# Kernel optimization log

Measured on AMD Instinct MI355X. Metric: run time of the kernel, lower is better.

The kernel has to match this reference:

```python
import jax, jax.numpy as jnp
import numpy as np

C = 256
NUM_HEADS = 4
GROUPS = 8
EPS = 1e-5


def setup_inputs() -> dict:
    key = jax.random.key(0)
    ks = jax.random.split(key, 7)
    B, H, W = 4, 64, 64
    x = jax.random.normal(ks[0], (B, C, H, W), dtype=jnp.float32)
    # GroupNorm affine params
    norm_w = jnp.ones((C,), dtype=jnp.float32)
    norm_b = jnp.zeros((C,), dtype=jnp.float32)
    # 1x1 convs == channel-mixing matrices
    qkv_w = jax.random.normal(ks[1], (3 * C, C), dtype=jnp.float32) * (C ** -0.5)
    qkv_b = jnp.zeros((3 * C,), dtype=jnp.float32)
    proj_w = jax.random.normal(ks[2], (C, C), dtype=jnp.float32) * (C ** -0.5)
    proj_b = jnp.zeros((C,), dtype=jnp.float32)
    return {"x": x, "norm_w": norm_w, "norm_b": norm_b,
            "qkv_w": qkv_w, "qkv_b": qkv_b,
            "proj_w": proj_w, "proj_b": proj_b}


def _group_norm(x, w, b):
    B, Cc, H, W = x.shape
    xr = x.reshape(B, GROUPS, Cc // GROUPS, H * W)
    mean = xr.mean(axis=(2, 3), keepdims=True)
    var = xr.var(axis=(2, 3), keepdims=True)
    xn = ((xr - mean) * jax.lax.rsqrt(var + EPS)).reshape(B, Cc, H, W)
    return xn * w[None, :, None, None] + b[None, :, None, None]


def reference(x, norm_w, norm_b, qkv_w, qkv_b, proj_w, proj_b):
    B, Cc, H, W = x.shape
    nh = NUM_HEADS
    d = Cc // nh
    h = _group_norm(x, norm_w, norm_b)
    # 1x1 conv: channel matmul
    qkv = jnp.einsum('oc,bchw->bohw', qkv_w, h) + qkv_b[None, :, None, None]
    q, k, v = jnp.split(qkv, 3, axis=1)
    q = q.reshape(B, nh, d, H * W)
    k = k.reshape(B, nh, d, H * W)
    v = v.reshape(B, nh, d, H * W)
    scale = d ** -0.5
    attn = jnp.einsum('bhci,bhcj->bhij', q, k) * scale  # [B, nh, HW, HW]
    attn = jax.nn.softmax(attn, axis=-1)
    o = jnp.einsum('bhij,bhcj->bhci', attn, v).reshape(B, Cc, H, W)
    out = jnp.einsum('oc,bchw->bohw', proj_w, o) + proj_b[None, :, None, None]
    return x + out
```

## Files before the change

### kernel.cpp

```cpp
#include <hip/hip_runtime.h>

typedef unsigned short u16;
typedef __attribute__((ext_vector_type(8))) short bf16x8;
typedef __attribute__((ext_vector_type(4))) float f32x4;
typedef __attribute__((ext_vector_type(16))) float f32x16;
typedef __attribute__((ext_vector_type(2))) int i32x2;

#define MFMA16(A, B, C) __builtin_amdgcn_mfma_f32_16x16x32_bf16((A), (B), (C), 0, 0, 0)
#define MFMA32(A, B, C) __builtin_amdgcn_mfma_f32_32x32x16_bf16((A), (B), (C), 0, 0, 0)

#define BB 4
#define CC 256
#define HW 4096
#define NH 4
#define HD 64

#define QSCALE 0.18033688f

__device__ __forceinline__ u16 f2bf(float f) {
  unsigned int u = __builtin_bit_cast(unsigned int, f);
  u += 0x7fffu + ((u >> 16) & 1u);
  return (u16)(u >> 16);
}

__device__ __forceinline__ unsigned cvtpk(float a, float b) {
  unsigned r;
  asm("v_cvt_pk_bf16_f32 %0, %1, %2" : "=v"(r) : "v"(a), "v"(b));
  return r;
}

__global__ __launch_bounds__(256) void w2bf_kernel(const float* __restrict__ qw,
                                                   const float* __restrict__ pw,
                                                   u16* __restrict__ wbf) {
  int idx = (blockIdx.x * 256 + threadIdx.x) * 4;
  const int NQ = 768 * 256;
  const float* src = (idx < NQ) ? (qw + idx) : (pw + (idx - NQ));
  float4 v = *(const float4*)src;
  union { u16 u[4]; uint2 w; } pk;
  pk.u[0] = f2bf(v.x); pk.u[1] = f2bf(v.y);
  pk.u[2] = f2bf(v.z); pk.u[3] = f2bf(v.w);
  *(uint2*)(wbf + idx) = pk.w;
}

__global__ __launch_bounds__(256) void gn_partial_kernel(const float* __restrict__ x,
                                                         float* __restrict__ partial) {
  const float4* p = (const float4*)(x + (size_t)blockIdx.x * 16384);
  float s = 0.f, ss = 0.f;
  for (int i = threadIdx.x; i < 4096; i += 256) {
    float4 v = p[i];
    s += (v.x + v.y) + (v.z + v.w);
    ss += (v.x * v.x + v.y * v.y) + (v.z * v.z + v.w * v.w);
  }
#pragma unroll
  for (int msk = 32; msk; msk >>= 1) {
    s += __shfl_xor(s, msk);
    ss += __shfl_xor(ss, msk);
  }
  __shared__ float red[2][4];
  int wave = threadIdx.x >> 6;
  if ((threadIdx.x & 63) == 0) { red[0][wave] = s; red[1][wave] = ss; }
  __syncthreads();
  if (threadIdx.x == 0) {
    partial[blockIdx.x] = red[0][0] + red[0][1] + red[0][2] + red[0][3];
    partial[256 + blockIdx.x] = red[1][0] + red[1][1] + red[1][2] + red[1][3];
  }
}

__global__ __launch_bounds__(64) void gn_final_kernel(const float* __restrict__ partial,
                                                      float* __restrict__ stats) {
  int bg = threadIdx.x;
  if (bg < 32) {
    float S = 0.f, SS = 0.f;
#pragma unroll
    for (int sp = 0; sp < 8; ++sp) {
      S += partial[bg * 8 + sp];
      SS += partial[256 + bg * 8 + sp];
    }
    const float invN = 1.0f / 131072.0f;
    float mean = S * invN;
    float var = SS * invN - mean * mean;
    stats[bg] = mean;
    stats[32 + bg] = rsqrtf(var + 1e-5f);
  }
}

__global__ __launch_bounds__(256) void norm_t_kernel(const float* __restrict__ x,
                                                     const float* __restrict__ nw,
                                                     const float* __restrict__ nb,
                                                     const float* __restrict__ stats,
                                                     u16* __restrict__ h_t) {
  int b = blockIdx.y;
  int s = blockIdx.x * 64 + (threadIdx.x & 63);
  int w = threadIdx.x >> 6;
  const float* xb = x + (size_t)b * CC * HW;
  u16* hb = h_t + ((size_t)b * HW + s) * CC;
#pragma unroll
  for (int cc = 0; cc < 8; ++cc) {
    int c0 = w * 64 + cc * 8;
    union { u16 u[8]; uint4 v; } pk;
#pragma unroll
    for (int j = 0; j < 8; ++j) {
      int c = c0 + j;
      int g = c >> 5;
      float mean = stats[b * 8 + g];
      float rstd = stats[32 + b * 8 + g];
      float a = nw[c] * rstd;
      float bb2 = nb[c] - mean * a;
      float vv = xb[(size_t)c * HW + s];
      pk.u[j] = f2bf(vv * a + bb2);
    }
    *(uint4*)(hb + c0) = pk.v;
  }
}

__global__ __launch_bounds__(256) void gemm_qk_kernel(const u16* __restrict__ h_t,
                                                      const u16* __restrict__ wbf,
                                                      const float* __restrict__ qb,
                                                      u16* __restrict__ q_t,
                                                      u16* __restrict__ k_f) {
  int b = blockIdx.z;
  int lane = threadIdx.x & 63, wave = threadIdx.x >> 6;
  int lr = lane & 15, lg = lane >> 4;
  int m0 = blockIdx.x * 128 + (wave >> 1) * 64;
  int n0 = blockIdx.y * 128 + (wave & 1) * 64;
  const u16* hb = h_t + (size_t)b * HW * CC;
  f32x4 acc[4][4] = {};
  for (int kc = 0; kc < 8; ++kc) {
    int ko = kc * 32 + lg * 8;
    bf16x8 af[4], bfr[4];
#pragma unroll
    for (int mi = 0; mi < 4; ++mi)
      af[mi] = *(const bf16x8*)(hb + (size_t)(m0 + mi * 16 + lr) * CC + ko);
#pragma unroll
    for (int ni = 0; ni < 4; ++ni)
      bfr[ni] = *(const bf16x8*)(wbf + (size_t)(n0 + ni * 16 + lr) * CC + ko);
#pragma unroll
    for (int mi = 0; mi < 4; ++mi)
#pragma unroll
      for (int ni = 0; ni < 4; ++ni)
        acc[mi][ni] = MFMA16(af[mi], bfr[ni], acc[mi][ni]);
  }
  bool isq = (blockIdx.y < 2);
  if (isq) {
#pragma unroll
    for (int ni = 0; ni < 4; ++ni) {
      int o = n0 + ni * 16 + lr;
      float bias = qb[o];
      u16* dp = q_t + (((size_t)b * NH + (o >> 6)) * HW) * HD + (o & 63);
#pragma unroll
      for (int mi = 0; mi < 4; ++mi)
#pragma unroll
        for (int r = 0; r < 4; ++r) {
          int s = m0 + mi * 16 + lg * 4 + r;
          dp[(size_t)s * HD] = f2bf((acc[mi][ni][r] + bias) * QSCALE);
        }
    }
  } else {
#pragma unroll
    for (int ni = 0; ni < 4; ++ni) {
      int o = n0 + ni * 16 + lr;
      int oc = o - 256;
      int h = oc >> 6, c = oc & 63;
      int kc = c >> 4, hi2 = (c >> 3) & 1, j = c & 7;
      float bias = qb[o];
      u16* base = k_f + (size_t)(b * NH + h) * HW * HD;
#pragma unroll
      for (int mi = 0; mi < 4; ++mi)
#pragma unroll
        for (int r = 0; r < 4; ++r) {
          int s = m0 + mi * 16 + lg * 4 + r;
          int jb32 = s >> 5, ql2 = s & 31;
          base[((size_t)(jb32 * 4 + kc) * 64 + hi2 * 32 + ql2) * 8 + j] =
              f2bf(acc[mi][ni][r] + bias);
        }
    }
  }
}

__global__ __launch_bounds__(256) void gemm_v_kernel(const u16* __restrict__ h_t,
                                                     const u16* __restrict__ wbf,
                                                     const float* __restrict__ qb,
                                                     u16* __restrict__ v_f) {
  int b = blockIdx.z;
  int lane = threadIdx.x & 63, wave = threadIdx.x >> 6;
  int lr = lane & 15, lg = lane >> 4;
  int m0 = blockIdx.y * 128 + (wave >> 1) * 64;
  int n0 = blockIdx.x * 128 + (wave & 1) * 64;
  const u16* hb = h_t + (size_t)b * HW * CC;
  f32x4 acc[4][4] = {};
  for (int kc = 0; kc < 8; ++kc) {
    int ko = kc * 32 + lg * 8;
    bf16x8 af[4], bfr[4];
#pragma unroll
    for (int mi = 0; mi < 4; ++mi)
      af[mi] = *(const bf16x8*)(wbf + (size_t)(512 + m0 + mi * 16 + lr) * CC + ko);
#pragma unroll
    for (int ni = 0; ni < 4; ++ni)
      bfr[ni] = *(const bf16x8*)(hb + (size_t)(n0 + ni * 16 + lr) * CC + ko);
#pragma unroll
    for (int mi = 0; mi < 4; ++mi)
#pragma unroll
      for (int ni = 0; ni < 4; ++ni)
        acc[mi][ni] = MFMA16(af[mi], bfr[ni], acc[mi][ni]);
  }
#pragma unroll
  for (int mi = 0; mi < 4; ++mi)
#pragma unroll
    for (int r = 0; r < 4; ++r) {
      int o = m0 + mi * 16 + lg * 4 + r;
      int h = o >> 6, c = o & 63;
      int half = c >> 5, qlc = c & 31;
      float bias = qb[512 + o];
      u16* base = v_f + (size_t)(b * NH + h) * HW * HD;
#pragma unroll
      for (int ni = 0; ni < 4; ++ni) {
        int s = n0 + ni * 16 + lr;
        int jb64 = s >> 6, w = s & 63;
        int kc = w >> 4, hi2 = (w >> 3) & 1, j = w & 7;
        base[((size_t)((jb64 * 2 + half) * 4 + kc) * 64 + hi2 * 32 + qlc) * 8 + j] =
            f2bf(acc[mi][ni][r] + bias);
      }
    }
}

__global__ __launch_bounds__(512) void attn_kernel(const u16* __restrict__ q_t,
                                                   const u16* __restrict__ k_f,
                                                   const u16* __restrict__ v_f,
                                                   u16* __restrict__ o_t) {
  __shared__ float mbuf[4 * 33 * 64];
  int wgid = blockIdx.x + gridDim.x * blockIdx.y;
  int xcd = wgid & 7;
  int j = wgid >> 3;
  int bh = (xcd << 1) | (j & 1);
  int qblk = j >> 1;
  int tid = threadIdx.x;
  int wave = tid >> 6, lane = tid & 63;
  int half = wave >> 2, wsub = wave & 3;
  int ql = lane & 31, hi = lane >> 5;
  int q0w = qblk * 128 + wsub * 32;
  const u16* qp = q_t + (size_t)bh * HW * HD;
  const u16* kfb = k_f + (size_t)bh * HW * HD + lane * 8;
  const u16* vfb = v_f + (size_t)bh * HW * HD + lane * 8;

  bf16x8 qf[4];
#pragma unroll
  for (int kc = 0; kc < 4; ++kc)
    qf[kc] = *(const bf16x8*)(qp + (size_t)(q0w + ql) * HD + kc * 16 + hi * 8);

  float l_run = 0.f;
  f32x16 of0 = {}, of1 = {};
  bf16x8 kfr[8], vfr[8];

  {
    const u16* kb = kfb + (size_t)half * 4096;
    const u16* vb = vfb + (size_t)half * 4096;
#pragma unroll
    for (int kc = 0; kc < 4; ++kc) {
      kfr[kc] = *(const bf16x8*)(kb + (size_t)kc * 512);
      kfr[4 + kc] = *(const bf16x8*)(kb + (size_t)(4 + kc) * 512);
      vfr[kc] = *(const bf16x8*)(vb + (size_t)kc * 512);
      vfr[4 + kc] = *(const bf16x8*)(vb + (size_t)(4 + kc) * 512);
    }
  }

#pragma unroll 1
  for (int it = half; it < 64; it += 2) {
    f32x16 s0 = {}, s1 = {};
    __builtin_amdgcn_s_setprio(1);
#pragma unroll
    for (int kc = 0; kc < 4; ++kc) {
      s0 = MFMA32(kfr[kc], qf[kc], s0);
      s1 = MFMA32(kfr[4 + kc], qf[kc], s1);
    }
    __builtin_amdgcn_s_setprio(0);

    {
      const u16* kb = kfb + (size_t)(it + 2) * 4096;
#pragma unroll
      for (int kc = 0; kc < 4; ++kc) {
        kfr[kc] = *(const bf16x8*)(kb + (size_t)kc * 512);
        kfr[4 + kc] = *(const bf16x8*)(kb + (size_t)(4 + kc) * 512);
      }
    }

#pragma unroll
    for (int i = 0; i < 16; ++i) {
      s0[i] = __builtin_amdgcn_exp2f(s0[i]);
      s1[i] = __builtin_amdgcn_exp2f(s1[i]);
    }

    bf16x8 pf[4];
#pragma unroll
    for (int kc = 0; kc < 4; ++kc) {
      const f32x16 pv = (kc < 2) ? s0 : s1;
      const int b8 = (kc & 1) * 8;
      unsigned A0 = cvtpk(pv[b8 + 0], pv[b8 + 1]);
      unsigned A1 = cvtpk(pv[b8 + 2], pv[b8 + 3]);
      unsigned B0 = cvtpk(pv[b8 + 4], pv[b8 + 5]);
      unsigned B1 = cvtpk(pv[b8 + 6], pv[b8 + 7]);
      i32x2 r0 = __builtin_amdgcn_permlane32_swap((int)A0, (int)B0, false, false);
      i32x2 r1 = __builtin_amdgcn_permlane32_swap((int)A1, (int)B1, false, false);
      union { unsigned w[4]; bf16x8 v8; } u;
      u.w[0] = (unsigned)r0[0]; u.w[1] = (unsigned)r1[0];
      u.w[2] = (unsigned)r0[1]; u.w[3] = (unsigned)r1[1];
      pf[kc] = u.v8;
    }

    __builtin_amdgcn_s_setprio(1);
#pragma unroll
    for (int kc = 0; kc < 4; ++kc) {
      of0 = MFMA32(vfr[kc], pf[kc], of0);
      of1 = MFMA32(vfr[4 + kc], pf[kc], of1);
    }
    __builtin_amdgcn_s_setprio(0);

    {
      const u16* vb = vfb + (size_t)(it + 2) * 4096;
#pragma unroll
      for (int kc = 0; kc < 4; ++kc) {
        vfr[kc] = *(const bf16x8*)(vb + (size_t)kc * 512);
        vfr[4 + kc] = *(const bf16x8*)(vb + (size_t)(4 + kc) * 512);
      }
    }

    float t8[8];
#pragma unroll
    for (int i = 0; i < 8; ++i)
      t8[i] = (s0[i] + s0[i + 8]) + (s1[i] + s1[i + 8]);
    float t4a = t8[0] + t8[4], t4b = t8[1] + t8[5];
    float t4c = t8[2] + t8[6], t4d = t8[3] + t8[7];
    l_run += (t4a + t4b) + (t4c + t4d);
  }

  __syncthreads();
  if (half == 1) {
    float* mb = mbuf + (size_t)wsub * 33 * 64 + lane;
#pragma unroll
    for (int i = 0; i < 16; ++i) mb[i * 64] = of0[i];
#pragma unroll
    for (int i = 0; i < 16; ++i) mb[(16 + i) * 64] = of1[i];
    mb[32 * 64] = l_run;
  }
  __syncthreads();
  if (half == 0) {
    const float* mb = mbuf + (size_t)wsub * 33 * 64 + lane;
#pragma unroll
    for (int i = 0; i < 16; ++i) of0[i] += mb[i * 64];
#pragma unroll
    for (int i = 0; i < 16; ++i) of1[i] += mb[(16 + i) * 64];
    l_run += mb[32 * 64];
    float l_tot = l_run + __shfl_xor(l_run, 32);
    float inv_l = 1.0f / l_tot;
    int bb = bh >> 2, hh = bh & 3;
    u16* orow = o_t + ((size_t)bb * HW + q0w + ql) * CC + hh * 64;
#pragma unroll
    for (int cb = 0; cb < 2; ++cb) {
      const f32x16 o = cb ? of1 : of0;
#pragma unroll
      for (int t = 0; t < 4; ++t) {
        int c0 = cb * 32 + t * 8 + hi * 4;
        union { u16 u[4]; uint2 w; } pk;
#pragma unroll
        for (int r = 0; r < 4; ++r) pk.u[r] = f2bf(o[t * 4 + r] * inv_l);
        *(uint2*)(orow + c0) = pk.w;
      }
    }
  }
}

__global__ __launch_bounds__(256) void proj_kernel(const u16* __restrict__ o_t,
                                                   const u16* __restrict__ wbf,
                                                   const float* __restrict__ pb,
                                                   const float* __restrict__ x,
                                                   float* __restrict__ out) {
  int b = blockIdx.z;
  int lane = threadIdx.x & 63, wave = threadIdx.x >> 6;
  int lr = lane & 15, lg = lane >> 4;
  int m0 = blockIdx.x * 128 + (wave >> 1) * 64;
  int n0 = blockIdx.y * 128 + (wave & 1) * 64;
  const u16* ob = o_t + (size_t)b * HW * CC;
  const u16* pwbf = wbf + (size_t)768 * CC;
  f32x4 acc[4][4] = {};
  for (int kc = 0; kc < 8; ++kc) {
    int ko = kc * 32 + lg * 8;
    bf16x8 af[4], bfr[4];
#pragma unroll
    for (int mi = 0; mi < 4; ++mi)
      af[mi] = *(const bf16x8*)(ob + (size_t)(m0 + mi * 16 + lr) * CC + ko);
#pragma unroll
    for (int ni = 0; ni < 4; ++ni)
      bfr[ni] = *(const bf16x8*)(pwbf + (size_t)(n0 + ni * 16 + lr) * CC + ko);
#pragma unroll
    for (int mi = 0; mi < 4; ++mi)
#pragma unroll
      for (int ni = 0; ni < 4; ++ni)
        acc[mi][ni] = MFMA16(af[mi], bfr[ni], acc[mi][ni]);
  }
#pragma unroll
  for (int ni = 0; ni < 4; ++ni) {
    int o = n0 + ni * 16 + lr;
    float bias = pb[o];
    const float* xp = x + ((size_t)b * CC + o) * HW;
    float* op = out + ((size_t)b * CC + o) * HW;
#pragma unroll
    for (int mi = 0; mi < 4; ++mi) {
      int sb = m0 + mi * 16 + lg * 4;
      float4 xv = *(const float4*)(xp + sb);
      float4 res;
      res.x = acc[mi][ni][0] + bias + xv.x;
      res.y = acc[mi][ni][1] + bias + xv.y;
      res.z = acc[mi][ni][2] + bias + xv.z;
      res.w = acc[mi][ni][3] + bias + xv.w;
      *(float4*)(op + sb) = res;
    }
  }
}

extern "C" void kernel_launch(void* const* d_in, const int* in_sizes, int n_in,
                              void* d_out, int out_size, void* d_ws, size_t ws_size,
                              hipStream_t stream) {
  const float* x = (const float*)d_in[0];
  const float* nw = (const float*)d_in[1];
  const float* nb = (const float*)d_in[2];
  const float* qw = (const float*)d_in[3];
  const float* qb = (const float*)d_in[4];
  const float* pw = (const float*)d_in[5];
  const float* pb = (const float*)d_in[6];
  float* out = (float*)d_out;

  float* stats = (float*)d_ws;
  float* partial = stats + 64;
  u16* h_t = (u16*)((char*)d_ws + 4096);
  u16* q_t = h_t + (size_t)BB * HW * CC;
  u16* k_f = q_t + (size_t)BB * HW * CC;
  u16* v_f = k_f + (size_t)BB * HW * CC;
  u16* wbf = v_f + (size_t)BB * HW * CC;
  u16* o_t = h_t;

  gn_partial_kernel<<<256, 256, 0, stream>>>(x, partial);
  gn_final_kernel<<<1, 64, 0, stream>>>(partial, stats);
  w2bf_kernel<<<256, 256, 0, stream>>>(qw, pw, wbf);
  norm_t_kernel<<<dim3(HW / 64, BB), 256, 0, stream>>>(x, nw, nb, stats, h_t);
  gemm_qk_kernel<<<dim3(HW / 128, 4, BB), 256, 0, stream>>>(h_t, wbf, qb, q_t, k_f);
  gemm_v_kernel<<<dim3(HW / 128, 2, BB), 256, 0, stream>>>(h_t, wbf, qb, v_f);
  attn_kernel<<<dim3(HW / 128, BB * NH), 512, 0, stream>>>(q_t, k_f, v_f, o_t);
  proj_kernel<<<dim3(HW / 128, 2, BB), 256, 0, stream>>>(o_t, wbf, pb, x, out);
}
```

Measured before the change: 155.6 us.

## Give each attention wave two query tiles to reuse K/V fragments

The attention kernel drops from 8 waves to 4 per block. Each wave now handles 64 queries as two 32-row tiles that share every loaded K and V fragment, and steps through 32-key chunks instead of 64. This halves the global K/V fragment loads per query and cuts the number of waves re-reading the same K/V. In exchange each wave holds more accumulator registers, which may lower occupancy, and the loop runs twice as many iterations.

```diff
diff --git a/kernel.cpp b/kernel.cpp
--- a/kernel.cpp
+++ b/kernel.cpp
@@ -223,11 +223,11 @@
     }
 }
 
-__global__ __launch_bounds__(512) void attn_kernel(const u16* __restrict__ q_t,
+__global__ __launch_bounds__(256) void attn_kernel(const u16* __restrict__ q_t,
                                                    const u16* __restrict__ k_f,
                                                    const u16* __restrict__ v_f,
                                                    u16* __restrict__ o_t) {
-  __shared__ float mbuf[4 * 33 * 64];
+  __shared__ float mbuf[2 * 66 * 64];
   int wgid = blockIdx.x + gridDim.x * blockIdx.y;
   int xcd = wgid & 7;
   int j = wgid >> 3;
@@ -235,134 +235,169 @@
   int qblk = j >> 1;
   int tid = threadIdx.x;
   int wave = tid >> 6, lane = tid & 63;
-  int half = wave >> 2, wsub = wave & 3;
+  int half = wave >> 1, qsel = wave & 1;
   int ql = lane & 31, hi = lane >> 5;
-  int q0w = qblk * 128 + wsub * 32;
+  int q0 = qblk * 128 + qsel * 64;
   const u16* qp = q_t + (size_t)bh * HW * HD;
   const u16* kfb = k_f + (size_t)bh * HW * HD + lane * 8;
   const u16* vfb = v_f + (size_t)bh * HW * HD + lane * 8;
 
-  bf16x8 qf[4];
-#pragma unroll
-  for (int kc = 0; kc < 4; ++kc)
-    qf[kc] = *(const bf16x8*)(qp + (size_t)(q0w + ql) * HD + kc * 16 + hi * 8);
-
-  float l_run = 0.f;
-  f32x16 of0 = {}, of1 = {};
-  bf16x8 kfr[8], vfr[8];
+  bf16x8 qfA[4], qfB[4];
+#pragma unroll
+  for (int kc = 0; kc < 4; ++kc) {
+    qfA[kc] = *(const bf16x8*)(qp + (size_t)(q0 + ql) * HD + kc * 16 + hi * 8);
+    qfB[kc] = *(const bf16x8*)(qp + (size_t)(q0 + 32 + ql) * HD + kc * 16 + hi * 8);
+  }
+
+  float lA = 0.f, lB = 0.f;
+  f32x16 oA0 = {}, oA1 = {}, oB0 = {}, oB1 = {};
+  bf16x8 kfr[4], vfr[4];
 
   {
-    const u16* kb = kfb + (size_t)half * 4096;
-    const u16* vb = vfb + (size_t)half * 4096;
+    const u16* kb = kfb + (size_t)(half * 4) * 512;
+#pragma unroll
+    for (int kc = 0; kc < 4; ++kc) kfr[kc] = *(const bf16x8*)(kb + (size_t)kc * 512);
+#pragma unroll
+    for (int h = 0; h < 2; ++h)
+#pragma unroll
+      for (int s = 0; s < 2; ++s)
+        vfr[h * 2 + s] = *(const bf16x8*)(vfb +
+            (size_t)(((half >> 1) * 2 + h) * 4 + (half & 1) * 2 + s) * 512);
+  }
+
+#pragma unroll 1
+  for (int g = half; g < 128; g += 2) {
+    f32x16 sA = {}, sB = {};
+    __builtin_amdgcn_s_setprio(1);
 #pragma unroll
     for (int kc = 0; kc < 4; ++kc) {
-      kfr[kc] = *(const bf16x8*)(kb + (size_t)kc * 512);
-      kfr[4 + kc] = *(const bf16x8*)(kb + (size_t)(4 + kc) * 512);
-      vfr[kc] = *(const bf16x8*)(vb + (size_t)kc * 512);
-      vfr[4 + kc] = *(const bf16x8*)(vb + (size_t)(4 + kc) * 512);
-    }
-  }
-
-#pragma unroll 1
-  for (int it = half; it < 64; it += 2) {
-    f32x16 s0 = {}, s1 = {};
-    __builtin_amdgcn_s_setprio(1);
-#pragma unroll
-    for (int kc = 0; kc < 4; ++kc) {
-      s0 = MFMA32(kfr[kc], qf[kc], s0);
-      s1 = MFMA32(kfr[4 + kc], qf[kc], s1);
+      sA = MFMA32(kfr[kc], qfA[kc], sA);
+      sB = MFMA32(kfr[kc], qfB[kc], sB);
     }
     __builtin_amdgcn_s_setprio(0);
 
-    {
-      const u16* kb = kfb + (size_t)(it + 2) * 4096;
-#pragma unroll
-      for (int kc = 0; kc < 4; ++kc) {
-        kfr[kc] = *(const bf16x8*)(kb + (size_t)kc * 512);
-        kfr[4 + kc] = *(const bf16x8*)(kb + (size_t)(4 + kc) * 512);
-      }
-    }
-
-#pragma unroll
-    for (int i = 0; i < 16; ++i) {
-      s0[i] = __builtin_amdgcn_exp2f(s0[i]);
-      s1[i] = __builtin_amdgcn_exp2f(s1[i]);
-    }
-
-    bf16x8 pf[4];
-#pragma unroll
-    for (int kc = 0; kc < 4; ++kc) {
-      const f32x16 pv = (kc < 2) ? s0 : s1;
-      const int b8 = (kc & 1) * 8;
-      unsigned A0 = cvtpk(pv[b8 + 0], pv[b8 + 1]);
-      unsigned A1 = cvtpk(pv[b8 + 2], pv[b8 + 3]);
-      unsigned B0 = cvtpk(pv[b8 + 4], pv[b8 + 5]);
-      unsigned B1 = cvtpk(pv[b8 + 6], pv[b8 + 7]);
+    if (g < 126) {
+      const u16* kb = kfb + (size_t)((g + 2) * 4) * 512;
+#pragma unroll
+      for (int kc = 0; kc < 4; ++kc) kfr[kc] = *(const bf16x8*)(kb + (size_t)kc * 512);
+    }
+
+#pragma unroll
+    for (int i = 0; i < 16; ++i) sA[i] = __builtin_amdgcn_exp2f(sA[i]);
+    bf16x8 pfA[2];
+#pragma unroll
+    for (int s = 0; s < 2; ++s) {
+      const int b8 = s * 8;
+      unsigned A0 = cvtpk(sA[b8 + 0], sA[b8 + 1]);
+      unsigned A1 = cvtpk(sA[b8 + 2], sA[b8 + 3]);
+      unsigned B0 = cvtpk(sA[b8 + 4], sA[b8 + 5]);
+      unsigned B1 = cvtpk(sA[b8 + 6], sA[b8 + 7]);
       i32x2 r0 = __builtin_amdgcn_permlane32_swap((int)A0, (int)B0, false, false);
       i32x2 r1 = __builtin_amdgcn_permlane32_swap((int)A1, (int)B1, false, false);
       union { unsigned w[4]; bf16x8 v8; } u;
       u.w[0] = (unsigned)r0[0]; u.w[1] = (unsigned)r1[0];
       u.w[2] = (unsigned)r0[1]; u.w[3] = (unsigned)r1[1];
-      pf[kc] = u.v8;
-    }
-
+      pfA[s] = u.v8;
+    }
     __builtin_amdgcn_s_setprio(1);
-#pragma unroll
-    for (int kc = 0; kc < 4; ++kc) {
-      of0 = MFMA32(vfr[kc], pf[kc], of0);
-      of1 = MFMA32(vfr[4 + kc], pf[kc], of1);
-    }
+    oA0 = MFMA32(vfr[0], pfA[0], oA0);
+    oA0 = MFMA32(vfr[1], pfA[1], oA0);
+    oA1 = MFMA32(vfr[2], pfA[0], oA1);
+    oA1 = MFMA32(vfr[3], pfA[1], oA1);
     __builtin_amdgcn_s_setprio(0);
 
+#pragma unroll
+    for (int i = 0; i < 16; ++i) sB[i] = __builtin_amdgcn_exp2f(sB[i]);
+    bf16x8 pfB[2];
+#pragma unroll
+    for (int s = 0; s < 2; ++s) {
+      const int b8 = s * 8;
+      unsigned A0 = cvtpk(sB[b8 + 0], sB[b8 + 1]);
+      unsigned A1 = cvtpk(sB[b8 + 2], sB[b8 + 3]);
+      unsigned B0 = cvtpk(sB[b8 + 4], sB[b8 + 5]);
+      unsigned B1 = cvtpk(sB[b8 + 6], sB[b8 + 7]);
+      i32x2 r0 = __builtin_amdgcn_permlane32_swap((int)A0, (int)B0, false, false);
+      i32x2 r1 = __builtin_amdgcn_permlane32_swap((int)A1, (int)B1, false, false);
+      union { unsigned w[4]; bf16x8 v8; } u;
+      u.w[0] = (unsigned)r0[0]; u.w[1] = (unsigned)r1[0];
+      u.w[2] = (unsigned)r0[1]; u.w[3] = (unsigned)r1[1];
+      pfB[s] = u.v8;
+    }
+    __builtin_amdgcn_s_setprio(1);
+    oB0 = MFMA32(vfr[0], pfB[0], oB0);
+    oB0 = MFMA32(vfr[1], pfB[1], oB0);
+    oB1 = MFMA32(vfr[2], pfB[0], oB1);
+    oB1 = MFMA32(vfr[3], pfB[1], oB1);
+    __builtin_amdgcn_s_setprio(0);
+
+    if (g < 126) {
+      int g2 = g + 2;
+#pragma unroll
+      for (int h = 0; h < 2; ++h)
+#pragma unroll
+        for (int s = 0; s < 2; ++s)
+          vfr[h * 2 + s] = *(const bf16x8*)(vfb +
+              (size_t)(((g2 >> 1) * 2 + h) * 4 + (g2 & 1) * 2 + s) * 512);
+    }
+
     {
-      const u16* vb = vfb + (size_t)(it + 2) * 4096;
-#pragma unroll
-      for (int kc = 0; kc < 4; ++kc) {
-        vfr[kc] = *(const bf16x8*)(vb + (size_t)kc * 512);
-        vfr[4 + kc] = *(const bf16x8*)(vb + (size_t)(4 + kc) * 512);
-      }
-    }
-
-    float t8[8];
-#pragma unroll
-    for (int i = 0; i < 8; ++i)
-      t8[i] = (s0[i] + s0[i + 8]) + (s1[i] + s1[i + 8]);
-    float t4a = t8[0] + t8[4], t4b = t8[1] + t8[5];
-    float t4c = t8[2] + t8[6], t4d = t8[3] + t8[7];
-    l_run += (t4a + t4b) + (t4c + t4d);
+      float t8[8];
+#pragma unroll
+      for (int i = 0; i < 8; ++i) t8[i] = sA[i] + sA[i + 8];
+      lA += ((t8[0] + t8[4]) + (t8[1] + t8[5])) + ((t8[2] + t8[6]) + (t8[3] + t8[7]));
+#pragma unroll
+      for (int i = 0; i < 8; ++i) t8[i] = sB[i] + sB[i + 8];
+      lB += ((t8[0] + t8[4]) + (t8[1] + t8[5])) + ((t8[2] + t8[6]) + (t8[3] + t8[7]));
+    }
   }
 
   __syncthreads();
   if (half == 1) {
-    float* mb = mbuf + (size_t)wsub * 33 * 64 + lane;
-#pragma unroll
-    for (int i = 0; i < 16; ++i) mb[i * 64] = of0[i];
-#pragma unroll
-    for (int i = 0; i < 16; ++i) mb[(16 + i) * 64] = of1[i];
-    mb[32 * 64] = l_run;
+    float* mb = mbuf + (size_t)qsel * 66 * 64 + lane;
+#pragma unroll
+    for (int i = 0; i < 16; ++i) mb[i * 64] = oA0[i];
+#pragma unroll
+    for (int i = 0; i < 16; ++i) mb[(16 + i) * 64] = oA1[i];
+#pragma unroll
+    for (int i = 0; i < 16; ++i) mb[(32 + i) * 64] = oB0[i];
+#pragma unroll
+    for (int i = 0; i < 16; ++i) mb[(48 + i) * 64] = oB1[i];
+    mb[64 * 64] = lA;
+    mb[65 * 64] = lB;
   }
   __syncthreads();
   if (half == 0) {
-    const float* mb = mbuf + (size_t)wsub * 33 * 64 + lane;
-#pragma unroll
-    for (int i = 0; i < 16; ++i) of0[i] += mb[i * 64];
-#pragma unroll
-    for (int i = 0; i < 16; ++i) of1[i] += mb[(16 + i) * 64];
-    l_run += mb[32 * 64];
-    float l_tot = l_run + __shfl_xor(l_run, 32);
-    float inv_l = 1.0f / l_tot;
+    const float* mb = mbuf + (size_t)qsel * 66 * 64 + lane;
+#pragma unroll
+    for (int i = 0; i < 16; ++i) oA0[i] += mb[i * 64];
+#pragma unroll
+    for (int i = 0; i < 16; ++i) oA1[i] += mb[(16 + i) * 64];
+#pragma unroll
+    for (int i = 0; i < 16; ++i) oB0[i] += mb[(32 + i) * 64];
+#pragma unroll
+    for (int i = 0; i < 16; ++i) oB1[i] += mb[(48 + i) * 64];
+    lA += mb[64 * 64];
+    lB += mb[65 * 64];
+    float lAt = lA + __shfl_xor(lA, 32);
+    float lBt = lB + __shfl_xor(lB, 32);
+    float invA = 1.0f / lAt;
+    float invB = 1.0f / lBt;
     int bb = bh >> 2, hh = bh & 3;
-    u16* orow = o_t + ((size_t)bb * HW + q0w + ql) * CC + hh * 64;
-#pragma unroll
-    for (int cb = 0; cb < 2; ++cb) {
-      const f32x16 o = cb ? of1 : of0;
-#pragma unroll
-      for (int t = 0; t < 4; ++t) {
-        int c0 = cb * 32 + t * 8 + hi * 4;
-        union { u16 u[4]; uint2 w; } pk;
-#pragma unroll
-        for (int r = 0; r < 4; ++r) pk.u[r] = f2bf(o[t * 4 + r] * inv_l);
-        *(uint2*)(orow + c0) = pk.w;
+#pragma unroll
+    for (int qs = 0; qs < 2; ++qs) {
+      float inv_l = qs ? invB : invA;
+      u16* orow = o_t + ((size_t)bb * HW + q0 + qs * 32 + ql) * CC + hh * 64;
+#pragma unroll
+      for (int cb = 0; cb < 2; ++cb) {
+        const f32x16 o = qs ? (cb ? oB1 : oB0) : (cb ? oA1 : oA0);
+#pragma unroll
+        for (int t = 0; t < 4; ++t) {
+          int c0 = cb * 32 + t * 8 + hi * 4;
+          union { u16 u[4]; uint2 w; } pk;
+#pragma unroll
+          for (int r = 0; r < 4; ++r) pk.u[r] = f2bf(o[t * 4 + r] * inv_l);
+          *(uint2*)(orow + c0) = pk.w;
+        }
       }
     }
   }
@@ -443,6 +478,6 @@
   norm_t_kernel<<<dim3(HW / 64, BB), 256, 0, stream>>>(x, nw, nb, stats, h_t);
   gemm_qk_kernel<<<dim3(HW / 128, 4, BB), 256, 0, stream>>>(h_t, wbf, qb, q_t, k_f);
   gemm_v_kernel<<<dim3(HW / 128, 2, BB), 256, 0, stream>>>(h_t, wbf, qb, v_f);
-  attn_kernel<<<dim3(HW / 128, BB * NH), 512, 0, stream>>>(q_t, k_f, v_f, o_t);
+  attn_kernel<<<dim3(HW / 128, BB * NH), 256, 0, stream>>>(q_t, k_f, v_f, o_t);
   proj_kernel<<<dim3(HW / 128, 2, BB), 256, 0, stream>>>(o_t, wbf, pb, x, out);
 }
```

After: 161.8 us. 4.0% more time.

## Fuse QK and V projection GEMMs into one 32x32 MFMA kernel with packed stores

Applied to the files above, without the earlier changes.

Merges the separate QK and V projection kernels into a single launch that uses 32x32x16 MFMA tiles. The bias is preloaded into the accumulators, and outputs are written as 16-byte packed fragments using permlane32 swaps, replacing scattered 2-byte stores. Q now goes into the same fragment layout as K, so the attention kernel loads Q with contiguous per-lane vectors. This is meant to cut launch overhead and the heavy scattered-store traffic in the projection epilogues, at the cost of a wider per-block branch between the Q/K and V paths.

```diff
diff --git a/kernel.cpp b/kernel.cpp
--- a/kernel.cpp
+++ b/kernel.cpp
@@ -2,12 +2,11 @@
 
 typedef unsigned short u16;
 typedef __attribute__((ext_vector_type(8))) short bf16x8;
-typedef __attribute__((ext_vector_type(4))) float f32x4;
 typedef __attribute__((ext_vector_type(16))) float f32x16;
 typedef __attribute__((ext_vector_type(2))) int i32x2;
 
+#define MFMA32(A, B, C) __builtin_amdgcn_mfma_f32_32x32x16_bf16((A), (B), (C), 0, 0, 0)
 #define MFMA16(A, B, C) __builtin_amdgcn_mfma_f32_16x16x32_bf16((A), (B), (C), 0, 0, 0)
-#define MFMA32(A, B, C) __builtin_amdgcn_mfma_f32_32x32x16_bf16((A), (B), (C), 0, 0, 0)
 
 #define BB 4
 #define CC 256
@@ -17,6 +16,8 @@
 
 #define QSCALE 0.18033688f
 
+typedef __attribute__((ext_vector_type(4))) float f32x4;
+
 __device__ __forceinline__ u16 f2bf(float f) {
   unsigned int u = __builtin_bit_cast(unsigned int, f);
   u += 0x7fffu + ((u >> 16) & 1u);
@@ -27,6 +28,20 @@
   unsigned r;
   asm("v_cvt_pk_bf16_f32 %0, %1, %2" : "=v"(r) : "v"(a), "v"(b));
   return r;
+}
+
+__device__ __forceinline__ uint4 pack_oct(const f32x16& a, int oct, float scl) {
+  const int b8 = oct * 8;
+  unsigned A0 = cvtpk(a[b8 + 0] * scl, a[b8 + 1] * scl);
+  unsigned A1 = cvtpk(a[b8 + 2] * scl, a[b8 + 3] * scl);
+  unsigned B0 = cvtpk(a[b8 + 4] * scl, a[b8 + 5] * scl);
+  unsigned B1 = cvtpk(a[b8 + 6] * scl, a[b8 + 7] * scl);
+  i32x2 r0 = __builtin_amdgcn_permlane32_swap((int)A0, (int)B0, false, false);
+  i32x2 r1 = __builtin_amdgcn_permlane32_swap((int)A1, (int)B1, false, false);
+  union { unsigned w[4]; uint4 v; } u;
+  u.w[0] = (unsigned)r0[0]; u.w[1] = (unsigned)r1[0];
+  u.w[2] = (unsigned)r0[1]; u.w[3] = (unsigned)r1[1];
+  return u.v;
 }
 
 __global__ __launch_bounds__(256) void w2bf_kernel(const float* __restrict__ qw,
@@ -113,117 +128,100 @@
   }
 }
 
-__global__ __launch_bounds__(256) void gemm_qk_kernel(const u16* __restrict__ h_t,
-                                                      const u16* __restrict__ wbf,
-                                                      const float* __restrict__ qb,
-                                                      u16* __restrict__ q_t,
-                                                      u16* __restrict__ k_f) {
+__global__ __launch_bounds__(256) void qkv_kernel(const u16* __restrict__ h_t,
+                                                  const u16* __restrict__ wbf,
+                                                  const float* __restrict__ qb,
+                                                  u16* __restrict__ q_f,
+                                                  u16* __restrict__ k_f,
+                                                  u16* __restrict__ v_f) {
   int b = blockIdx.z;
+  int y = blockIdx.y;
   int lane = threadIdx.x & 63, wave = threadIdx.x >> 6;
-  int lr = lane & 15, lg = lane >> 4;
-  int m0 = blockIdx.x * 128 + (wave >> 1) * 64;
-  int n0 = blockIdx.y * 128 + (wave & 1) * 64;
+  int ql = lane & 31, hi = lane >> 5;
+  int s0w = blockIdx.x * 128 + (wave >> 1) * 64;
+  int o0w = y * 128 + (wave & 1) * 64;
+  bool isV = (y >= 4);
   const u16* hb = h_t + (size_t)b * HW * CC;
-  f32x4 acc[4][4] = {};
-  for (int kc = 0; kc < 8; ++kc) {
-    int ko = kc * 32 + lg * 8;
-    bf16x8 af[4], bfr[4];
-#pragma unroll
-    for (int mi = 0; mi < 4; ++mi)
-      af[mi] = *(const bf16x8*)(hb + (size_t)(m0 + mi * 16 + lr) * CC + ko);
-#pragma unroll
-    for (int ni = 0; ni < 4; ++ni)
-      bfr[ni] = *(const bf16x8*)(wbf + (size_t)(n0 + ni * 16 + lr) * CC + ko);
-#pragma unroll
-    for (int mi = 0; mi < 4; ++mi)
-#pragma unroll
-      for (int ni = 0; ni < 4; ++ni)
-        acc[mi][ni] = MFMA16(af[mi], bfr[ni], acc[mi][ni]);
-  }
-  bool isq = (blockIdx.y < 2);
-  if (isq) {
-#pragma unroll
-    for (int ni = 0; ni < 4; ++ni) {
-      int o = n0 + ni * 16 + lr;
-      float bias = qb[o];
-      u16* dp = q_t + (((size_t)b * NH + (o >> 6)) * HW) * HD + (o & 63);
-#pragma unroll
-      for (int mi = 0; mi < 4; ++mi)
-#pragma unroll
-        for (int r = 0; r < 4; ++r) {
-          int s = m0 + mi * 16 + lg * 4 + r;
-          dp[(size_t)s * HD] = f2bf((acc[mi][ni][r] + bias) * QSCALE);
+
+  f32x16 acc[2][2];
+  if (!isV) {
+#pragma unroll
+    for (int mo = 0; mo < 2; ++mo)
+#pragma unroll
+      for (int r = 0; r < 16; ++r) {
+        int row = (r & 3) + 8 * (r >> 2) + 4 * hi;
+        float bv = qb[o0w + mo * 32 + row];
+        acc[mo][0][r] = bv;
+        acc[mo][1][r] = bv;
+      }
+  } else {
+#pragma unroll
+    for (int ns = 0; ns < 2; ++ns) {
+      float bv = qb[o0w + ns * 32 + ql];
+#pragma unroll
+      for (int r = 0; r < 16; ++r) {
+        acc[0][ns][r] = bv;
+        acc[1][ns][r] = bv;
+      }
+    }
+  }
+
+  for (int kk = 0; kk < 16; ++kk) {
+    int k0 = kk * 16 + hi * 8;
+    bf16x8 wf[2], hf[2];
+#pragma unroll
+    for (int t = 0; t < 2; ++t) {
+      wf[t] = *(const bf16x8*)(wbf + (size_t)(o0w + t * 32 + ql) * CC + k0);
+      hf[t] = *(const bf16x8*)(hb + (size_t)(s0w + t * 32 + ql) * CC + k0);
+    }
+    if (!isV) {
+      acc[0][0] = MFMA32(wf[0], hf[0], acc[0][0]);
+      acc[0][1] = MFMA32(wf[0], hf[1], acc[0][1]);
+      acc[1][0] = MFMA32(wf[1], hf[0], acc[1][0]);
+      acc[1][1] = MFMA32(wf[1], hf[1], acc[1][1]);
+    } else {
+      acc[0][0] = MFMA32(hf[0], wf[0], acc[0][0]);
+      acc[0][1] = MFMA32(hf[0], wf[1], acc[0][1]);
+      acc[1][0] = MFMA32(hf[1], wf[0], acc[1][0]);
+      acc[1][1] = MFMA32(hf[1], wf[1], acc[1][1]);
+    }
+  }
+
+  if (!isV) {
+    bool isQ = (y < 2);
+    float scl = isQ ? QSCALE : 1.0f;
+    int headL = (o0w >> 6) - (isQ ? 0 : 4);
+    u16* base = (isQ ? q_f : k_f) + (size_t)(b * NH + headL) * HW * HD;
+#pragma unroll
+    for (int mo = 0; mo < 2; ++mo)
+#pragma unroll
+      for (int ns = 0; ns < 2; ++ns) {
+        int s32 = (s0w >> 5) + ns;
+#pragma unroll
+        for (int oct = 0; oct < 2; ++oct) {
+          int kc = mo * 2 + oct;
+          uint4 v = pack_oct(acc[mo][ns], oct, scl);
+          *(uint4*)(base + ((size_t)(s32 * 4 + kc) * 64 + lane) * 8) = v;
         }
-    }
+      }
   } else {
-#pragma unroll
-    for (int ni = 0; ni < 4; ++ni) {
-      int o = n0 + ni * 16 + lr;
-      int oc = o - 256;
-      int h = oc >> 6, c = oc & 63;
-      int kc = c >> 4, hi2 = (c >> 3) & 1, j = c & 7;
-      float bias = qb[o];
-      u16* base = k_f + (size_t)(b * NH + h) * HW * HD;
-#pragma unroll
-      for (int mi = 0; mi < 4; ++mi)
-#pragma unroll
-        for (int r = 0; r < 4; ++r) {
-          int s = m0 + mi * 16 + lg * 4 + r;
-          int jb32 = s >> 5, ql2 = s & 31;
-          base[((size_t)(jb32 * 4 + kc) * 64 + hi2 * 32 + ql2) * 8 + j] =
-              f2bf(acc[mi][ni][r] + bias);
+    int headv = (o0w >> 6) - 8;
+    u16* base = v_f + (size_t)(b * NH + headv) * HW * HD;
+#pragma unroll
+    for (int mo = 0; mo < 2; ++mo)
+#pragma unroll
+      for (int ns = 0; ns < 2; ++ns)
+#pragma unroll
+        for (int oct = 0; oct < 2; ++oct) {
+          int kvb = s0w + mo * 32 + oct * 16;
+          int jb64 = kvb >> 6, kcv = (kvb & 63) >> 4;
+          uint4 v = pack_oct(acc[mo][ns], oct, 1.0f);
+          *(uint4*)(base + ((size_t)((jb64 * 2 + ns) * 4 + kcv) * 64 + lane) * 8) = v;
         }
-    }
-  }
-}
-
-__global__ __launch_bounds__(256) void gemm_v_kernel(const u16* __restrict__ h_t,
-                                                     const u16* __restrict__ wbf,
-                                                     const float* __restrict__ qb,
-                                                     u16* __restrict__ v_f) {
-  int b = blockIdx.z;
-  int lane = threadIdx.x & 63, wave = threadIdx.x >> 6;
-  int lr = lane & 15, lg = lane >> 4;
-  int m0 = blockIdx.y * 128 + (wave >> 1) * 64;
-  int n0 = blockIdx.x * 128 + (wave & 1) * 64;
-  const u16* hb = h_t + (size_t)b * HW * CC;
-  f32x4 acc[4][4] = {};
-  for (int kc = 0; kc < 8; ++kc) {
-    int ko = kc * 32 + lg * 8;
-    bf16x8 af[4], bfr[4];
-#pragma unroll
-    for (int mi = 0; mi < 4; ++mi)
-      af[mi] = *(const bf16x8*)(wbf + (size_t)(512 + m0 + mi * 16 + lr) * CC + ko);
-#pragma unroll
-    for (int ni = 0; ni < 4; ++ni)
-      bfr[ni] = *(const bf16x8*)(hb + (size_t)(n0 + ni * 16 + lr) * CC + ko);
-#pragma unroll
-    for (int mi = 0; mi < 4; ++mi)
-#pragma unroll
-      for (int ni = 0; ni < 4; ++ni)
-        acc[mi][ni] = MFMA16(af[mi], bfr[ni], acc[mi][ni]);
-  }
-#pragma unroll
-  for (int mi = 0; mi < 4; ++mi)
-#pragma unroll
-    for (int r = 0; r < 4; ++r) {
-      int o = m0 + mi * 16 + lg * 4 + r;
-      int h = o >> 6, c = o & 63;
-      int half = c >> 5, qlc = c & 31;
-      float bias = qb[512 + o];
-      u16* base = v_f + (size_t)(b * NH + h) * HW * HD;
-#pragma unroll
-      for (int ni = 0; ni < 4; ++ni) {
-        int s = n0 + ni * 16 + lr;
-        int jb64 = s >> 6, w = s & 63;
-        int kc = w >> 4, hi2 = (w >> 3) & 1, j = w & 7;
-        base[((size_t)((jb64 * 2 + half) * 4 + kc) * 64 + hi2 * 32 + qlc) * 8 + j] =
-            f2bf(acc[mi][ni][r] + bias);
-      }
-    }
-}
-
-__global__ __launch_bounds__(512) void attn_kernel(const u16* __restrict__ q_t,
+  }
+}
+
+__global__ __launch_bounds__(512) void attn_kernel(const u16* __restrict__ q_f,
                                                    const u16* __restrict__ k_f,
                                                    const u16* __restrict__ v_f,
                                                    u16* __restrict__ o_t) {
@@ -238,14 +236,15 @@
   int half = wave >> 2, wsub = wave & 3;
   int ql = lane & 31, hi = lane >> 5;
   int q0w = qblk * 128 + wsub * 32;
-  const u16* qp = q_t + (size_t)bh * HW * HD;
+  const u16* qfb = q_f + (size_t)bh * HW * HD + lane * 8;
   const u16* kfb = k_f + (size_t)bh * HW * HD + lane * 8;
   const u16* vfb = v_f + (size_t)bh * HW * HD + lane * 8;
 
+  int s32q = q0w >> 5;
   bf16x8 qf[4];
 #pragma unroll
   for (int kc = 0; kc < 4; ++kc)
-    qf[kc] = *(const bf16x8*)(qp + (size_t)(q0w + ql) * HD + kc * 16 + hi * 8);
+    qf[kc] = *(const bf16x8*)(qfb + (size_t)(s32q * 4 + kc) * 512);
 
   float l_run = 0.f;
   f32x16 of0 = {}, of1 = {};
@@ -431,8 +430,8 @@
   float* stats = (float*)d_ws;
   float* partial = stats + 64;
   u16* h_t = (u16*)((char*)d_ws + 4096);
-  u16* q_t = h_t + (size_t)BB * HW * CC;
-  u16* k_f = q_t + (size_t)BB * HW * CC;
+  u16* q_f = h_t + (size_t)BB * HW * CC;
+  u16* k_f = q_f + (size_t)BB * HW * CC;
   u16* v_f = k_f + (size_t)BB * HW * CC;
   u16* wbf = v_f + (size_t)BB * HW * CC;
   u16* o_t = h_t;
@@ -441,8 +440,7 @@
   gn_final_kernel<<<1, 64, 0, stream>>>(partial, stats);
   w2bf_kernel<<<256, 256, 0, stream>>>(qw, pw, wbf);
   norm_t_kernel<<<dim3(HW / 64, BB), 256, 0, stream>>>(x, nw, nb, stats, h_t);
-  gemm_qk_kernel<<<dim3(HW / 128, 4, BB), 256, 0, stream>>>(h_t, wbf, qb, q_t, k_f);
-  gemm_v_kernel<<<dim3(HW / 128, 2, BB), 256, 0, stream>>>(h_t, wbf, qb, v_f);
-  attn_kernel<<<dim3(HW / 128, BB * NH), 512, 0, stream>>>(q_t, k_f, v_f, o_t);
+  qkv_kernel<<<dim3(HW / 128, 6, BB), 256, 0, stream>>>(h_t, wbf, qb, q_f, k_f, v_f);
+  attn_kernel<<<dim3(HW / 128, BB * NH), 512, 0, stream>>>(q_f, k_f, v_f, o_t);
   proj_kernel<<<dim3(HW / 128, 2, BB), 256, 0, stream>>>(o_t, wbf, pb, x, out);
 }
```

Result: no change. 154.5 us (-0.7%).
